# Optimization experiments

Measured on AMD Instinct MI355X. Metric: run time of the kernel, lower is better.

The kernel has to match this reference:

```python
import jax, jax.numpy as jnp
import numpy as np

B, N, F_IN = 4, 2048, 256
K, D = 4, 64
NEG_SLOPE = 0.2


def setup_inputs() -> dict:
    key = jax.random.key(0)
    k1, k2, k3, k4, k5 = jax.random.split(key, 5)
    x = jax.random.normal(k1, (B, N, F_IN), dtype=jnp.float32)
    adj = jax.random.randint(k2, (B, N, N), 0, 2, dtype=jnp.int32)
    # xavier_uniform-style params
    def xavier(k, shape):
        fan_in, fan_out = shape[-2], shape[-1]
        lim = np.sqrt(6.0 / (fan_in + fan_out))
        return jax.random.uniform(k, shape, jnp.float32, -lim, lim)
    W = xavier(k3, (K, F_IN, D))
    a_src = xavier(k4, (K, D, 1))
    a_dst = xavier(k5, (K, D, 1))
    return {"x": x, "adj": adj, "W": W, "a_src": a_src, "a_dst": a_dst}


def reference(x, adj, W, a_src, a_dst):
    # Wh: (B, K, N, D)
    Wh = jnp.einsum('bnf,kfd->bknd', x, W)
    e_src = jnp.einsum('bknd,kdo->bkno', Wh, a_src)  # (B,K,N,1)
    e_dst = jnp.einsum('bknd,kdo->bkno', Wh, a_dst)  # (B,K,N,1)
    e = e_src + jnp.swapaxes(e_dst, -2, -1)          # (B,K,N,N)
    e = jnp.where(e > 0, e, NEG_SLOPE * e)           # LeakyReLU(0.2)
    # adjacency mask with forced self-loops (adj + I > 0)
    eye = jnp.eye(e.shape[-1], dtype=bool)
    mask = (adj[:, None, :, :] > 0) | eye            # (B,1|K,N,N)
    e = jnp.where(mask, e, -jnp.inf)
    # numerically-stable softmax matching F_module_softmax
    x_max = jnp.max(e, axis=-1, keepdims=True)
    x_max = jnp.where(jnp.isinf(x_max), 0.0, x_max)
    exp_e = jnp.exp(e - x_max)
    exp_e = jnp.where(jnp.isinf(e), 0.0, exp_e)
    alpha = exp_e / (jnp.sum(exp_e, axis=-1, keepdims=True) + 1e-10)
    # dropout is identity in eval mode
    out = jnp.matmul(alpha, Wh)                      # (B,K,N,D)
    # concat heads: (B,N,K*D)
    Bn, Kn, Nn, Dn = out.shape
    return jnp.transpose(out, (0, 2, 1, 3)).reshape(Bn, Nn, Kn * Dn)
```

## Files before the change

kernel.cpp:

```cpp
#include <hip/hip_runtime.h>

#define NB 4
#define NN 2048
#define NF 256
#define NK 4
#define ND 64
#define NEG 0.2f
#define LOG2E 1.4426950408889634f

typedef _Float16 f16;
typedef _Float16 f16x2 __attribute__((ext_vector_type(2)));
typedef _Float16 f16x4 __attribute__((ext_vector_type(4)));
typedef _Float16 f16x8 __attribute__((ext_vector_type(8)));
typedef float f32x4 __attribute__((ext_vector_type(4)));
typedef float f32x16 __attribute__((ext_vector_type(16)));
typedef unsigned int u32;
typedef unsigned short u16;

__device__ __forceinline__ int gsz(int d) { return (d ^ (d >> 3)) & 7; }

__global__ __launch_bounds__(256) void k01(
    const float* __restrict__ x,
    const int*   __restrict__ adj,
    const float* __restrict__ Wm,
    const float* __restrict__ a_src,
    const float* __restrict__ a_dst,
    unsigned int* __restrict__ abit,
    f16* __restrict__ wht,
    float* __restrict__ sbuf,
    f16* __restrict__ ebuf,
    f16* __restrict__ fbuf)
{
    __shared__ f16 wt[64 * 256];

    const int bx  = blockIdx.x;
    const int tid = threadIdx.x;

    if (bx >= 256) {
        const int row = (bx - 256) * 4 + (tid >> 6);
        const int l   = tid & 63;
        const int i   = row & (NN - 1);
        const int* __restrict__ ar = adj + (size_t)row * NN;

        int v[32];
#pragma unroll
        for (int c = 0; c < 32; ++c) v[c] = ar[c * 64 + l];

        unsigned int kx = 0, ky = 0;
#pragma unroll
        for (int c = 0; c < 32; ++c) {
            unsigned long long m = __ballot(v[c] > 0);
            if (l == c) { kx = (unsigned int)m; ky = (unsigned int)(m >> 32); }
        }
        if (l == (i >> 6)) {
            unsigned int sb = 1u << (i & 31);
            if (((i >> 5) & 1) == 0) kx |= sb; else ky |= sb;
        }
        if (l < 32) {
            uint2 kk; kk.x = kx; kk.y = ky;
            *(uint2*)&abit[(size_t)row * 64 + l * 2] = kk;
        }
        return;
    }

    const int gx  = bx & 15;
    const int k   = (bx >> 4) & 3;
    const int b   = bx >> 6;
    const int wv  = tid >> 6;
    const int l   = tid & 63;
    const int q   = l >> 4;
    const int r16 = l & 15;

    for (int fc = 0; fc < 64; ++fc) {
        int f = fc * 4 + wv;
        int d = l;
        wt[d * 256 + (f ^ ((d & 7) << 3))] = (f16)Wm[(k * NF + f) * ND + d];
    }
    __syncthreads();

    const int ncol0 = gx * 128 + wv * 32;
    f32x4 acc[2][4];
#pragma unroll
    for (int nt = 0; nt < 2; ++nt)
#pragma unroll
        for (int dt = 0; dt < 4; ++dt)
            acc[nt][dt] = (f32x4){0.f, 0.f, 0.f, 0.f};

    for (int fs = 0; fs < 16; ++fs) {
        const int f0 = fs * 16 + q * 4;
        f16x4 af[4];
#pragma unroll
        for (int dt = 0; dt < 4; ++dt) {
            int d = dt * 16 + r16;
            af[dt] = *(const f16x4*)&wt[d * 256 + (f0 ^ ((d & 7) << 3))];
        }
#pragma unroll
        for (int nt = 0; nt < 2; ++nt) {
            int n = ncol0 + nt * 16 + r16;
            float4 xv = *(const float4*)&x[((size_t)(b * NN + n)) * NF + f0];
            f16x4 bf = {(f16)xv.x, (f16)xv.y, (f16)xv.z, (f16)xv.w};
#pragma unroll
            for (int dt = 0; dt < 4; ++dt)
                acc[nt][dt] = __builtin_amdgcn_mfma_f32_16x16x16f16(
                    af[dt], bf, acc[nt][dt], 0, 0, 0);
        }
    }

    float asv[4][4], adv[4][4];
#pragma unroll
    for (int dt = 0; dt < 4; ++dt)
#pragma unroll
        for (int rr = 0; rr < 4; ++rr) {
            int d = dt * 16 + q * 4 + rr;
            asv[dt][rr] = a_src[k * ND + d];
            adv[dt][rr] = a_dst[k * ND + d];
        }

    const size_t obase = (size_t)(b * NK + k) * 131072;

#pragma unroll
    for (int nt = 0; nt < 2; ++nt) {
        int n  = ncol0 + nt * 16 + r16;
        int s_ = n >> 6, g = (n >> 3) & 7, e = n & 7;
        float sp = 0.f, tp = 0.f;
#pragma unroll
        for (int dt = 0; dt < 4; ++dt)
#pragma unroll
            for (int rr = 0; rr < 4; ++rr) {
                float v = acc[nt][dt][rr];
                int d = dt * 16 + q * 4 + rr;
                wht[obase + s_ * 4096 + d * 64 + ((g ^ gsz(d)) << 3) + e] = (f16)v;
                sp += v * asv[dt][rr];
                tp += v * adv[dt][rr];
            }
        sp += __shfl_xor(sp, 16);
        sp += __shfl_xor(sp, 32);
        tp += __shfl_xor(tp, 16);
        tp += __shfl_xor(tp, 32);
        if (q == 0) {
            int idx = (b * NK + k) * NN + n;
            sbuf[idx] = sp;
            ebuf[idx] = (f16)__builtin_exp2f(tp * LOG2E);
            fbuf[idx] = (f16)__builtin_exp2f(0.2f * LOG2E * tp);
        }
    }
}

__global__ __launch_bounds__(512, 4) void k2_attn(
    const unsigned int* __restrict__ abit,
    const f16* __restrict__ wht,
    const float* __restrict__ sbuf,
    const f16* __restrict__ ebuf,
    const f16* __restrict__ fbuf,
    float* __restrict__ out)
{
    const int i0  = blockIdx.x * 64;
    const int k   = blockIdx.y;
    const int b   = blockIdx.z;
    const int tid = threadIdx.x;
    const int w   = tid >> 6;
    const int c   = w >> 1;
    const int rw  = w & 1;
    const int l   = tid & 63;
    const int r32 = l & 31;
    const int hi  = l >> 5;
    const int iglob = i0 + rw * 32 + r32;

    __shared__ __attribute__((aligned(16))) char pool[74752];
    u16*   el   = (u16*)(pool + 65536);
    u16*   fl   = (u16*)(pool + 69632);
    float* dden = (float*)(pool + 73728);

    const unsigned int* __restrict__ abrow =
        abit + (size_t)(b * NN + iglob) * 64 + c * 16;
    uint2 abx[8];
#pragma unroll
    for (int it = 0; it < 8; ++it) abx[it] = *(const uint2*)(abrow + it * 2);

    {
        const u16* eb = (const u16*)(ebuf + (b * NK + k) * NN);
        const u16* fb = (const u16*)(fbuf + (b * NK + k) * NN);
        *(ushort4*)&el[tid * 4] = *(const ushort4*)&eb[tid * 4];
        *(ushort4*)&fl[tid * 4] = *(const ushort4*)&fb[tid * 4];
    }

    const float s   = sbuf[(b * NK + k) * NN + iglob];
    const float Aff = __builtin_exp2f(0.8f * LOG2E * fminf(s, 0.f));
    const float Bff = __builtin_exp2f(-0.8f * LOG2E * fmaxf(s, 0.f));
    const f16 Afh = (f16)Aff, Bfh = (f16)Bff;
    const f16x2 Af2 = {Afh, Afh};
    const f16x2 Bf2 = {Bfh, Bfh};
    const f16x2 one2 = {(f16)1.0f, (f16)1.0f};
    const char* gtiles = (const char*)wht + (size_t)(b * NK + k) * 262144;

    float denom = 0.f;
    f32x16 acc[2];
#pragma unroll
    for (int dh = 0; dh < 2; ++dh)
#pragma unroll
        for (int z = 0; z < 16; ++z) acc[dh][z] = 0.f;

#define STAGE8(bb, it)                                                         \
    do {                                                                       \
        const char* gsrc = gtiles + (size_t)(c * 8 + (it)) * 8192 +            \
                           rw * 1024 + l * 16;                                 \
        char* ldst = pool + c * 16384 + (bb) * 8192 + rw * 1024 + l * 16;      \
        _Pragma("unroll") for (int kk = 0; kk < 4; ++kk)                       \
            __builtin_amdgcn_global_load_lds(                                  \
                (const __attribute__((address_space(1))) void*)(gsrc +         \
                    kk * 2048),                                                \
                (__attribute__((address_space(3))) void*)(ldst + kk * 2048),   \
                16, 0, 0);                                                     \
    } while (0)

    STAGE8(0, 0);

#pragma unroll
    for (int it = 0; it < 8; ++it) {
        asm volatile("s_waitcnt vmcnt(0) lgkmcnt(0)" ::: "memory");
        __builtin_amdgcn_sched_barrier(0);
        __builtin_amdgcn_s_barrier();
        __builtin_amdgcn_sched_barrier(0);
        if (it < 7) STAGE8((it + 1) & 1, it + 1);

        const char* lb = pool + c * 16384 + (it & 1) * 8192;
        const uint2 ab = abx[it];
#pragma unroll
        for (int jts = 0; jts < 4; ++jts) {
            const u32 word = (jts & 2) ? ab.y : ab.x;
            const u32 bbyte = (word >> (((jts & 1) << 4) + (hi << 3))) & 0xffu;
            const u32 u = bbyte * 0x8001u;
            const int jb = c * 512 + it * 64 + jts * 16 + hi * 8;
            uint4 E4 = *(const uint4*)&el[jb];
            uint4 F4 = *(const uint4*)&fl[jb];
            u32 pa_u[4];
#pragma unroll
            for (int p = 0; p < 4; ++p) {
                f16x2 e2 = __builtin_bit_cast(f16x2, ((const u32*)&E4)[p]);
                f16x2 f2 = __builtin_bit_cast(f16x2, ((const u32*)&F4)[p]);
                f16x2 w2 = __builtin_elementwise_max(Af2 * e2, Bf2 * f2);
                u32 x  = (u >> (2 * p)) & 0x00010001u;
                u32 mm = x * 0xffffu;
                u32 wu = __builtin_bit_cast(u32, w2) & mm;
                pa_u[p] = wu;
                denom = __builtin_amdgcn_fdot2(
                    __builtin_bit_cast(f16x2, wu), one2, denom, false);
            }
            uint4 pav = {pa_u[0], pa_u[1], pa_u[2], pa_u[3]};
            f16x8 pa = __builtin_bit_cast(f16x8, pav);
#pragma unroll
            for (int dh = 0; dh < 2; ++dh) {
                const int d = dh * 32 + r32;
                f16x8 v8 = *(const f16x8*)(lb + d * 128 +
                               ((((jts << 1) | hi) ^ gsz(d)) << 4));
                acc[dh] = __builtin_amdgcn_mfma_f32_32x32x16_f16(
                    pa, v8, acc[dh], 0, 0, 0);
            }
        }
    }
#undef STAGE8

    denom += __shfl_xor(denom, 32);

    __syncthreads();
    float* stash = (float*)pool;
    if (c != 0) {
        float* sb = stash + ((c - 1) * 2 + rw) * 2048 + l * 32;
#pragma unroll
        for (int dh = 0; dh < 2; ++dh)
#pragma unroll
            for (int sub = 0; sub < 4; ++sub) {
                f32x4 v = {acc[dh][sub * 4], acc[dh][sub * 4 + 1],
                           acc[dh][sub * 4 + 2], acc[dh][sub * 4 + 3]};
                *(f32x4*)&sb[dh * 16 + ((sub ^ (l & 3)) << 2)] = v;
            }
    }
    if (hi == 0) dden[c * 64 + rw * 32 + r32] = denom;
    __syncthreads();

    if (c == 0) {
#pragma unroll
        for (int cc = 0; cc < 3; ++cc) {
            const float* sr = stash + (cc * 2 + rw) * 2048 + l * 32;
#pragma unroll
            for (int dh = 0; dh < 2; ++dh)
#pragma unroll
                for (int sub = 0; sub < 4; ++sub) {
                    f32x4 v = *(const f32x4*)&sr[dh * 16 + ((sub ^ (l & 3)) << 2)];
#pragma unroll
                    for (int m = 0; m < 4; ++m) acc[dh][sub * 4 + m] += v[m];
                }
        }
        float* op = out + ((size_t)(b * NN) + i0 + rw * 32) * (NK * ND) + k * ND;
#pragma unroll
        for (int g4 = 0; g4 < 4; ++g4) {
            f32x4 ds = {0.f, 0.f, 0.f, 0.f};
#pragma unroll
            for (int c4 = 0; c4 < 4; ++c4) {
                f32x4 dv = *(const f32x4*)&dden[c4 * 64 + rw * 32 + g4 * 8 + hi * 4];
#pragma unroll
                for (int m = 0; m < 4; ++m) ds[m] += dv[m];
            }
#pragma unroll
            for (int m = 0; m < 4; ++m) {
                const int rr   = g4 * 4 + m;
                const int irow = g4 * 8 + hi * 4 + m;
                const float inv = 1.f / (ds[m] + 1e-10f);
                op[(size_t)irow * (NK * ND) + r32]      = acc[0][rr] * inv;
                op[(size_t)irow * (NK * ND) + 32 + r32] = acc[1][rr] * inv;
            }
        }
    }
}

extern "C" void kernel_launch(void* const* d_in, const int* in_sizes, int n_in,
                              void* d_out, int out_size, void* d_ws, size_t ws_size,
                              hipStream_t stream) {
    const float* x     = (const float*)d_in[0];
    const int*   adj   = (const int*)d_in[1];
    const float* Wm    = (const float*)d_in[2];
    const float* a_src = (const float*)d_in[3];
    const float* a_dst = (const float*)d_in[4];
    float* out = (float*)d_out;

    char* ws = (char*)d_ws;
    f16*   wht  = (f16*)ws;
    float* sbuf = (float*)(ws + (4u << 20));
    f16*   ebuf = (f16*)(ws + (4u << 20) + (128u << 10));
    f16*   fbuf = (f16*)(ws + (4u << 20) + (192u << 10));
    unsigned int* abit = (unsigned int*)(ws + (4u << 20) + (256u << 10));

    k01<<<dim3(256 + NB * NN / 4), 256, 0, stream>>>(
        x, adj, Wm, a_src, a_dst, abit, wht, sbuf, ebuf, fbuf);
    k2_attn<<<dim3(NN / 64, NK, NB), 512, 0, stream>>>(
        abit, wht, sbuf, ebuf, fbuf, out);
}
```

Measured before the change: 42.71 us.

## Split attention key range across all eight waves with per-wave pipelines and tree reduction

The attention kernel changes from 4 key-chunks × 2 row-halves to 8 waves that each own a 256-key slice and compute both 32-row tiles. Each V fragment loaded from LDS is now reused for two MFMAs. Each wave stages its own Wh tiles with a double-buffered global_load_lds pipeline using partial vmcnt waits, which removes the per-iteration workgroup barrier. The Wh tile layout and swizzle are changed to 32-column slabs to match, the grid is flattened so blocks sharing the same (b,k) run adjacently, and the cross-wave sum becomes a log-depth LDS tree reduction. The cost is more accumulator registers, because acc doubles, and a longer reduction epilogue.

```diff
diff --git a/kernel.cpp b/kernel.cpp
--- a/kernel.cpp
+++ b/kernel.cpp
@@ -17,7 +17,7 @@
 typedef unsigned int u32;
 typedef unsigned short u16;
 
-__device__ __forceinline__ int gsz(int d) { return (d ^ (d >> 3)) & 7; }
+__device__ __forceinline__ int gq(int d) { return ((d >> 1) ^ (d >> 3)) & 3; }
 
 __global__ __launch_bounds__(256) void k01(
     const float* __restrict__ x,
@@ -121,7 +121,7 @@
 #pragma unroll
     for (int nt = 0; nt < 2; ++nt) {
         int n  = ncol0 + nt * 16 + r16;
-        int s_ = n >> 6, g = (n >> 3) & 7, e = n & 7;
+        int s_ = n >> 5, g = (n >> 3) & 3, e = n & 7;
         float sp = 0.f, tp = 0.f;
 #pragma unroll
         for (int dt = 0; dt < 4; ++dt)
@@ -129,7 +129,7 @@
             for (int rr = 0; rr < 4; ++rr) {
                 float v = acc[nt][dt][rr];
                 int d = dt * 16 + q * 4 + rr;
-                wht[obase + s_ * 4096 + d * 64 + ((g ^ gsz(d)) << 3) + e] = (f16)v;
+                wht[obase + s_ * 2048 + d * 32 + ((g ^ gq(d)) << 3) + e] = (f16)v;
                 sp += v * asv[dt][rr];
                 tp += v * adv[dt][rr];
             }
@@ -154,163 +154,200 @@
     const f16* __restrict__ fbuf,
     float* __restrict__ out)
 {
-    const int i0  = blockIdx.x * 64;
-    const int k   = blockIdx.y;
-    const int b   = blockIdx.z;
+    const int bid = blockIdx.x;
+    const int bkv = (bid & 7) | (((bid >> 3) & 1) << 3);
+    const int rg  = bid >> 4;
+    const int b   = bkv >> 2, k = bkv & 3;
     const int tid = threadIdx.x;
     const int w   = tid >> 6;
-    const int c   = w >> 1;
-    const int rw  = w & 1;
     const int l   = tid & 63;
     const int r32 = l & 31;
     const int hi  = l >> 5;
-    const int iglob = i0 + rw * 32 + r32;
-
-    __shared__ __attribute__((aligned(16))) char pool[74752];
+    const int rowbase = rg * 64;
+
+    __shared__ __attribute__((aligned(16))) char pool[76032];
     u16*   el   = (u16*)(pool + 65536);
     u16*   fl   = (u16*)(pool + 69632);
     float* dden = (float*)(pool + 73728);
-
-    const unsigned int* __restrict__ abrow =
-        abit + (size_t)(b * NN + iglob) * 64 + c * 16;
-    uint2 abx[8];
-#pragma unroll
-    for (int it = 0; it < 8; ++it) abx[it] = *(const uint2*)(abrow + it * 2);
+    float* dsum = (float*)(pool + 75776);
+
+    const unsigned int* ab0 = abit + (size_t)(b * NN + rowbase + r32) * 64 + w * 8;
+    const unsigned int* ab1 = ab0 + 32 * 64;
+    uint2 abxA[4], abxB[4];
+#pragma unroll
+    for (int xw = 0; xw < 4; ++xw) {
+        abxA[xw] = *(const uint2*)(ab0 + xw * 2);
+        abxB[xw] = *(const uint2*)(ab1 + xw * 2);
+    }
+    const float s0 = sbuf[bkv * NN + rowbase + r32];
+    const float s1 = sbuf[bkv * NN + rowbase + 32 + r32];
 
     {
-        const u16* eb = (const u16*)(ebuf + (b * NK + k) * NN);
-        const u16* fb = (const u16*)(fbuf + (b * NK + k) * NN);
-        *(ushort4*)&el[tid * 4] = *(const ushort4*)&eb[tid * 4];
-        *(ushort4*)&fl[tid * 4] = *(const ushort4*)&fb[tid * 4];
-    }
-
-    const float s   = sbuf[(b * NK + k) * NN + iglob];
-    const float Aff = __builtin_exp2f(0.8f * LOG2E * fminf(s, 0.f));
-    const float Bff = __builtin_exp2f(-0.8f * LOG2E * fmaxf(s, 0.f));
-    const f16 Afh = (f16)Aff, Bfh = (f16)Bff;
-    const f16x2 Af2 = {Afh, Afh};
-    const f16x2 Bf2 = {Bfh, Bfh};
+        const u16* eb = (const u16*)(ebuf + bkv * NN);
+        const u16* fb = (const u16*)(fbuf + bkv * NN);
+        *(uint2*)&el[tid * 4] = *(const uint2*)&eb[tid * 4];
+        *(uint2*)&fl[tid * 4] = *(const uint2*)&fb[tid * 4];
+    }
+
+    const f16 Af0h = (f16)__builtin_exp2f(0.8f * LOG2E * fminf(s0, 0.f));
+    const f16 Bf0h = (f16)__builtin_exp2f(-0.8f * LOG2E * fmaxf(s0, 0.f));
+    const f16 Af1h = (f16)__builtin_exp2f(0.8f * LOG2E * fminf(s1, 0.f));
+    const f16 Bf1h = (f16)__builtin_exp2f(-0.8f * LOG2E * fmaxf(s1, 0.f));
+    const f16x2 Af2[2] = {{Af0h, Af0h}, {Af1h, Af1h}};
+    const f16x2 Bf2[2] = {{Bf0h, Bf0h}, {Bf1h, Bf1h}};
     const f16x2 one2 = {(f16)1.0f, (f16)1.0f};
-    const char* gtiles = (const char*)wht + (size_t)(b * NK + k) * 262144;
-
-    float denom = 0.f;
-    f32x16 acc[2];
-#pragma unroll
-    for (int dh = 0; dh < 2; ++dh)
-#pragma unroll
-        for (int z = 0; z < 16; ++z) acc[dh][z] = 0.f;
-
-#define STAGE8(bb, it)                                                         \
+    const char* gtb = (const char*)wht + (size_t)bkv * 262144;
+
+    const int G0 = ((r32 >> 1) ^ (r32 >> 3)) & 3;
+    const int G1 = (((32 + r32) >> 1) ^ ((32 + r32) >> 3)) & 3;
+    const int fb0 = r32 * 64;
+    const int fb1 = 2048 + r32 * 64;
+
+    float den0 = 0.f, den1 = 0.f;
+    f32x16 acc[2][2];
+#pragma unroll
+    for (int rt = 0; rt < 2; ++rt)
+#pragma unroll
+        for (int dh = 0; dh < 2; ++dh)
+#pragma unroll
+            for (int z = 0; z < 16; ++z) acc[rt][dh][z] = 0.f;
+
+#define STAGE(bb, it)                                                          \
     do {                                                                       \
-        const char* gsrc = gtiles + (size_t)(c * 8 + (it)) * 8192 +            \
-                           rw * 1024 + l * 16;                                 \
-        char* ldst = pool + c * 16384 + (bb) * 8192 + rw * 1024 + l * 16;      \
+        const char* gsrc = gtb + (size_t)(w * 8 + (it)) * 4096 + l * 16;       \
+        char* ldst = pool + w * 8192 + (bb) * 4096;                            \
         _Pragma("unroll") for (int kk = 0; kk < 4; ++kk)                       \
             __builtin_amdgcn_global_load_lds(                                  \
                 (const __attribute__((address_space(1))) void*)(gsrc +         \
-                    kk * 2048),                                                \
-                (__attribute__((address_space(3))) void*)(ldst + kk * 2048),   \
+                    kk * 1024),                                                \
+                (__attribute__((address_space(3))) void*)(ldst + kk * 1024),   \
                 16, 0, 0);                                                     \
     } while (0)
 
-    STAGE8(0, 0);
+    STAGE(0, 0);
+    STAGE(1, 1);
+    __syncthreads();
 
 #pragma unroll
     for (int it = 0; it < 8; ++it) {
-        asm volatile("s_waitcnt vmcnt(0) lgkmcnt(0)" ::: "memory");
+        if (it < 7) asm volatile("s_waitcnt vmcnt(4)" ::: "memory");
+        else        asm volatile("s_waitcnt vmcnt(0)" ::: "memory");
         __builtin_amdgcn_sched_barrier(0);
-        __builtin_amdgcn_s_barrier();
+
+        const char* lb = pool + w * 8192 + (it & 1) * 4096;
+        const int j0 = w * 256 + it * 32;
+        const u32 wordA = (it & 1) ? abxA[it >> 1].y : abxA[it >> 1].x;
+        const u32 wordB = (it & 1) ? abxB[it >> 1].y : abxB[it >> 1].x;
+
+#pragma unroll
+        for (int jts = 0; jts < 2; ++jts) {
+            const int v = (jts << 1) | hi;
+            uint4 E4 = *(const uint4*)&el[j0 + jts * 16 + hi * 8];
+            uint4 F4 = *(const uint4*)&fl[j0 + jts * 16 + hi * 8];
+            f16x8 v8_0 = *(const f16x8*)(lb + fb0 + ((v ^ G0) << 4));
+            f16x8 v8_1 = *(const f16x8*)(lb + fb1 + ((v ^ G1) << 4));
+
+            f16x8 pa[2];
+#pragma unroll
+            for (int rt = 0; rt < 2; ++rt) {
+                const u32 word = rt ? wordB : wordA;
+                const u32 bbyte = (word >> ((jts << 4) + (hi << 3))) & 0xffu;
+                const u32 u = bbyte * 0x8001u;
+                u32 pa_u[4];
+#pragma unroll
+                for (int p = 0; p < 4; ++p) {
+                    f16x2 e2 = __builtin_bit_cast(f16x2, ((const u32*)&E4)[p]);
+                    f16x2 f2 = __builtin_bit_cast(f16x2, ((const u32*)&F4)[p]);
+                    f16x2 w2 = __builtin_elementwise_max(Af2[rt] * e2,
+                                                         Bf2[rt] * f2);
+                    u32 mm = ((u >> (2 * p)) & 0x00010001u) * 0xffffu;
+                    u32 wu = __builtin_bit_cast(u32, w2) & mm;
+                    pa_u[p] = wu;
+                    float& dref = rt ? den1 : den0;
+                    dref = __builtin_amdgcn_fdot2(
+                        __builtin_bit_cast(f16x2, wu), one2, dref, false);
+                }
+                uint4 pav = {pa_u[0], pa_u[1], pa_u[2], pa_u[3]};
+                pa[rt] = __builtin_bit_cast(f16x8, pav);
+            }
+            acc[0][0] = __builtin_amdgcn_mfma_f32_32x32x16_f16(pa[0], v8_0,
+                                                               acc[0][0], 0, 0, 0);
+            acc[0][1] = __builtin_amdgcn_mfma_f32_32x32x16_f16(pa[0], v8_1,
+                                                               acc[0][1], 0, 0, 0);
+            acc[1][0] = __builtin_amdgcn_mfma_f32_32x32x16_f16(pa[1], v8_0,
+                                                               acc[1][0], 0, 0, 0);
+            acc[1][1] = __builtin_amdgcn_mfma_f32_32x32x16_f16(pa[1], v8_1,
+                                                               acc[1][1], 0, 0, 0);
+        }
+        asm volatile("s_waitcnt lgkmcnt(0)" ::: "memory");
         __builtin_amdgcn_sched_barrier(0);
-        if (it < 7) STAGE8((it + 1) & 1, it + 1);
-
-        const char* lb = pool + c * 16384 + (it & 1) * 8192;
-        const uint2 ab = abx[it];
-#pragma unroll
-        for (int jts = 0; jts < 4; ++jts) {
-            const u32 word = (jts & 2) ? ab.y : ab.x;
-            const u32 bbyte = (word >> (((jts & 1) << 4) + (hi << 3))) & 0xffu;
-            const u32 u = bbyte * 0x8001u;
-            const int jb = c * 512 + it * 64 + jts * 16 + hi * 8;
-            uint4 E4 = *(const uint4*)&el[jb];
-            uint4 F4 = *(const uint4*)&fl[jb];
-            u32 pa_u[4];
-#pragma unroll
-            for (int p = 0; p < 4; ++p) {
-                f16x2 e2 = __builtin_bit_cast(f16x2, ((const u32*)&E4)[p]);
-                f16x2 f2 = __builtin_bit_cast(f16x2, ((const u32*)&F4)[p]);
-                f16x2 w2 = __builtin_elementwise_max(Af2 * e2, Bf2 * f2);
-                u32 x  = (u >> (2 * p)) & 0x00010001u;
-                u32 mm = x * 0xffffu;
-                u32 wu = __builtin_bit_cast(u32, w2) & mm;
-                pa_u[p] = wu;
-                denom = __builtin_amdgcn_fdot2(
-                    __builtin_bit_cast(f16x2, wu), one2, denom, false);
-            }
-            uint4 pav = {pa_u[0], pa_u[1], pa_u[2], pa_u[3]};
-            f16x8 pa = __builtin_bit_cast(f16x8, pav);
-#pragma unroll
-            for (int dh = 0; dh < 2; ++dh) {
-                const int d = dh * 32 + r32;
-                f16x8 v8 = *(const f16x8*)(lb + d * 128 +
-                               ((((jts << 1) | hi) ^ gsz(d)) << 4));
-                acc[dh] = __builtin_amdgcn_mfma_f32_32x32x16_f16(
-                    pa, v8, acc[dh], 0, 0, 0);
-            }
-        }
-    }
-#undef STAGE8
-
-    denom += __shfl_xor(denom, 32);
-
-    __syncthreads();
-    float* stash = (float*)pool;
-    if (c != 0) {
-        float* sb = stash + ((c - 1) * 2 + rw) * 2048 + l * 32;
-#pragma unroll
-        for (int dh = 0; dh < 2; ++dh)
-#pragma unroll
-            for (int sub = 0; sub < 4; ++sub) {
-                f32x4 v = {acc[dh][sub * 4], acc[dh][sub * 4 + 1],
-                           acc[dh][sub * 4 + 2], acc[dh][sub * 4 + 3]};
-                *(f32x4*)&sb[dh * 16 + ((sub ^ (l & 3)) << 2)] = v;
-            }
-    }
-    if (hi == 0) dden[c * 64 + rw * 32 + r32] = denom;
-    __syncthreads();
-
-    if (c == 0) {
-#pragma unroll
-        for (int cc = 0; cc < 3; ++cc) {
-            const float* sr = stash + (cc * 2 + rw) * 2048 + l * 32;
-#pragma unroll
-            for (int dh = 0; dh < 2; ++dh)
-#pragma unroll
-                for (int sub = 0; sub < 4; ++sub) {
-                    f32x4 v = *(const f32x4*)&sr[dh * 16 + ((sub ^ (l & 3)) << 2)];
-#pragma unroll
-                    for (int m = 0; m < 4; ++m) acc[dh][sub * 4 + m] += v[m];
+        if (it < 6) STAGE(it & 1, it + 2);
+    }
+#undef STAGE
+
+    den0 += __shfl_xor(den0, 32);
+    den1 += __shfl_xor(den1, 32);
+    if (hi == 0) {
+        dden[w * 64 + r32]      = den0;
+        dden[w * 64 + 32 + r32] = den1;
+    }
+
+#define TDUMP(reg)                                                             \
+    do {                                                                       \
+        float* rb = (float*)(pool + (reg) * 16384) + l * 64;                   \
+        _Pragma("unroll") for (int rt = 0; rt < 2; ++rt)                       \
+        _Pragma("unroll") for (int dh = 0; dh < 2; ++dh)                       \
+        _Pragma("unroll") for (int sub = 0; sub < 4; ++sub) {                  \
+            f32x4 vv = {acc[rt][dh][sub * 4], acc[rt][dh][sub * 4 + 1],        \
+                        acc[rt][dh][sub * 4 + 2], acc[rt][dh][sub * 4 + 3]};   \
+            *(f32x4*)&rb[((rt * 8 + dh * 4 + sub) ^ (l & 15)) << 2] = vv;      \
+        }                                                                      \
+    } while (0)
+#define TADD(reg)                                                              \
+    do {                                                                       \
+        const float* rb = (const float*)(pool + (reg) * 16384) + l * 64;       \
+        _Pragma("unroll") for (int rt = 0; rt < 2; ++rt)                       \
+        _Pragma("unroll") for (int dh = 0; dh < 2; ++dh)                       \
+        _Pragma("unroll") for (int sub = 0; sub < 4; ++sub) {                  \
+            f32x4 vv = *(const f32x4*)                                         \
+                &rb[((rt * 8 + dh * 4 + sub) ^ (l & 15)) << 2];                \
+            _Pragma("unroll") for (int m = 0; m < 4; ++m)                      \
+                acc[rt][dh][sub * 4 + m] += vv[m];                             \
+        }                                                                      \
+    } while (0)
+
+    __syncthreads();
+    if (w >= 4) TDUMP(w - 4);
+    __syncthreads();
+    if (w < 4) TADD(w);
+    if (w == 2 || w == 3) TDUMP(w);
+    __syncthreads();
+    if (w < 2) TADD(w + 2);
+    if (w == 1) TDUMP(1);
+    __syncthreads();
+    if (w == 0) {
+        TADD(1);
+        float dd8 = 0.f;
+#pragma unroll
+        for (int ww = 0; ww < 8; ++ww) dd8 += dden[ww * 64 + l];
+        dsum[l] = dd8;
+        float* ob = out + ((size_t)(b * NN) + rowbase) * (NK * ND) + k * ND;
+#pragma unroll
+        for (int rt = 0; rt < 2; ++rt)
+#pragma unroll
+            for (int g4 = 0; g4 < 4; ++g4)
+#pragma unroll
+                for (int m = 0; m < 4; ++m) {
+                    const int rowl = rt * 32 + g4 * 8 + hi * 4 + m;
+                    const float inv = 1.f / (dsum[rowl] + 1e-10f);
+                    const int rr = g4 * 4 + m;
+                    ob[(size_t)rowl * (NK * ND) + r32] = acc[rt][0][rr] * inv;
+                    ob[(size_t)rowl * (NK * ND) + 32 + r32] =
+                        acc[rt][1][rr] * inv;
                 }
-        }
-        float* op = out + ((size_t)(b * NN) + i0 + rw * 32) * (NK * ND) + k * ND;
-#pragma unroll
-        for (int g4 = 0; g4 < 4; ++g4) {
-            f32x4 ds = {0.f, 0.f, 0.f, 0.f};
-#pragma unroll
-            for (int c4 = 0; c4 < 4; ++c4) {
-                f32x4 dv = *(const f32x4*)&dden[c4 * 64 + rw * 32 + g4 * 8 + hi * 4];
-#pragma unroll
-                for (int m = 0; m < 4; ++m) ds[m] += dv[m];
-            }
-#pragma unroll
-            for (int m = 0; m < 4; ++m) {
-                const int rr   = g4 * 4 + m;
-                const int irow = g4 * 8 + hi * 4 + m;
-                const float inv = 1.f / (ds[m] + 1e-10f);
-                op[(size_t)irow * (NK * ND) + r32]      = acc[0][rr] * inv;
-                op[(size_t)irow * (NK * ND) + 32 + r32] = acc[1][rr] * inv;
-            }
-        }
-    }
+    }
+#undef TDUMP
+#undef TADD
 }
 
 extern "C" void kernel_launch(void* const* d_in, const int* in_sizes, int n_in,
@@ -332,6 +369,6 @@
 
     k01<<<dim3(256 + NB * NN / 4), 256, 0, stream>>>(
         x, adj, Wm, a_src, a_dst, abit, wht, sbuf, ebuf, fbuf);
-    k2_attn<<<dim3(NN / 64, NK, NB), 512, 0, stream>>>(
+    k2_attn<<<dim3(512), 512, 0, stream>>>(
         abit, wht, sbuf, ebuf, fbuf, out);
 }
```

After: 68.47 us. +60.3%, slower.

## Compute softmax denominator via MFMA with ones and remap grid to 1D

Applied to the files above, without the earlier changes.

Replaces the per-element fdot2 denominator accumulation with an extra MFMA against a ones matrix, so row sums come out in the accumulator layout and the separate denominator LDS buffer and shuffle go away. The attention kernel grid becomes 1D, with block IDs interleaving the 16 (batch, head) pairs fastest so that concurrently resident blocks spread across heads and batches. It also simplifies the mask construction with shifts and stashes the denominator tile alongside the partial accumulators. The cost is one more MFMA per step and a larger stash in shared memory.

```diff
diff --git a/kernel.cpp b/kernel.cpp
--- a/kernel.cpp
+++ b/kernel.cpp
@@ -154,9 +154,11 @@
     const f16* __restrict__ fbuf,
     float* __restrict__ out)
 {
-    const int i0  = blockIdx.x * 64;
-    const int k   = blockIdx.y;
-    const int b   = blockIdx.z;
+    const int bid = blockIdx.x;
+    const int bkv = (bid & 7) | (((bid >> 3) & 1) << 3);
+    const int rg  = bid >> 4;
+    const int b   = bkv >> 2, k = bkv & 3;
+    const int i0  = rg * 64;
     const int tid = threadIdx.x;
     const int w   = tid >> 6;
     const int c   = w >> 1;
@@ -167,9 +169,8 @@
     const int iglob = i0 + rw * 32 + r32;
 
     __shared__ __attribute__((aligned(16))) char pool[74752];
-    u16*   el   = (u16*)(pool + 65536);
-    u16*   fl   = (u16*)(pool + 69632);
-    float* dden = (float*)(pool + 73728);
+    u16* el = (u16*)(pool + 65536);
+    u16* fl = (u16*)(pool + 69632);
 
     const unsigned int* __restrict__ abrow =
         abit + (size_t)(b * NN + iglob) * 64 + c * 16;
@@ -178,27 +179,24 @@
     for (int it = 0; it < 8; ++it) abx[it] = *(const uint2*)(abrow + it * 2);
 
     {
-        const u16* eb = (const u16*)(ebuf + (b * NK + k) * NN);
-        const u16* fb = (const u16*)(fbuf + (b * NK + k) * NN);
+        const u16* eb = (const u16*)(ebuf + bkv * NN);
+        const u16* fb = (const u16*)(fbuf + bkv * NN);
         *(ushort4*)&el[tid * 4] = *(const ushort4*)&eb[tid * 4];
         *(ushort4*)&fl[tid * 4] = *(const ushort4*)&fb[tid * 4];
     }
 
-    const float s   = sbuf[(b * NK + k) * NN + iglob];
-    const float Aff = __builtin_exp2f(0.8f * LOG2E * fminf(s, 0.f));
-    const float Bff = __builtin_exp2f(-0.8f * LOG2E * fmaxf(s, 0.f));
-    const f16 Afh = (f16)Aff, Bfh = (f16)Bff;
+    const float s   = sbuf[bkv * NN + iglob];
+    const f16 Afh = (f16)__builtin_exp2f(0.8f * LOG2E * fminf(s, 0.f));
+    const f16 Bfh = (f16)__builtin_exp2f(-0.8f * LOG2E * fmaxf(s, 0.f));
     const f16x2 Af2 = {Afh, Afh};
     const f16x2 Bf2 = {Bfh, Bfh};
-    const f16x2 one2 = {(f16)1.0f, (f16)1.0f};
-    const char* gtiles = (const char*)wht + (size_t)(b * NK + k) * 262144;
-
-    float denom = 0.f;
-    f32x16 acc[2];
-#pragma unroll
-    for (int dh = 0; dh < 2; ++dh)
-#pragma unroll
-        for (int z = 0; z < 16; ++z) acc[dh][z] = 0.f;
+    const f16 h1 = (f16)1.0f;
+    const f16x8 ones8 = {h1, h1, h1, h1, h1, h1, h1, h1};
+    const char* gtiles = (const char*)wht + (size_t)bkv * 262144;
+
+    f32x16 acc[2], accd;
+#pragma unroll
+    for (int z = 0; z < 16; ++z) { acc[0][z] = 0.f; acc[1][z] = 0.f; accd[z] = 0.f; }
 
 #define STAGE8(bb, it)                                                         \
     do {                                                                       \
@@ -229,7 +227,7 @@
         for (int jts = 0; jts < 4; ++jts) {
             const u32 word = (jts & 2) ? ab.y : ab.x;
             const u32 bbyte = (word >> (((jts & 1) << 4) + (hi << 3))) & 0xffu;
-            const u32 u = bbyte * 0x8001u;
+            const u32 u = (bbyte << 15) | bbyte;
             const int jb = c * 512 + it * 64 + jts * 16 + hi * 8;
             uint4 E4 = *(const uint4*)&el[jb];
             uint4 F4 = *(const uint4*)&fl[jb];
@@ -240,11 +238,8 @@
                 f16x2 f2 = __builtin_bit_cast(f16x2, ((const u32*)&F4)[p]);
                 f16x2 w2 = __builtin_elementwise_max(Af2 * e2, Bf2 * f2);
                 u32 x  = (u >> (2 * p)) & 0x00010001u;
-                u32 mm = x * 0xffffu;
-                u32 wu = __builtin_bit_cast(u32, w2) & mm;
-                pa_u[p] = wu;
-                denom = __builtin_amdgcn_fdot2(
-                    __builtin_bit_cast(f16x2, wu), one2, denom, false);
+                u32 mm = (x << 16) - x;
+                pa_u[p] = __builtin_bit_cast(u32, w2) & mm;
             }
             uint4 pav = {pa_u[0], pa_u[1], pa_u[2], pa_u[3]};
             f16x8 pa = __builtin_bit_cast(f16x8, pav);
@@ -256,16 +251,15 @@
                 acc[dh] = __builtin_amdgcn_mfma_f32_32x32x16_f16(
                     pa, v8, acc[dh], 0, 0, 0);
             }
+            accd = __builtin_amdgcn_mfma_f32_32x32x16_f16(pa, ones8, accd, 0, 0, 0);
         }
     }
 #undef STAGE8
-
-    denom += __shfl_xor(denom, 32);
 
     __syncthreads();
     float* stash = (float*)pool;
     if (c != 0) {
-        float* sb = stash + ((c - 1) * 2 + rw) * 2048 + l * 32;
+        float* sb = stash + ((c - 1) * 2 + rw) * 3072 + l * 48;
 #pragma unroll
         for (int dh = 0; dh < 2; ++dh)
 #pragma unroll
@@ -274,14 +268,19 @@
                            acc[dh][sub * 4 + 2], acc[dh][sub * 4 + 3]};
                 *(f32x4*)&sb[dh * 16 + ((sub ^ (l & 3)) << 2)] = v;
             }
-    }
-    if (hi == 0) dden[c * 64 + rw * 32 + r32] = denom;
+#pragma unroll
+        for (int sub = 0; sub < 4; ++sub) {
+            f32x4 v = {accd[sub * 4], accd[sub * 4 + 1],
+                       accd[sub * 4 + 2], accd[sub * 4 + 3]};
+            *(f32x4*)&sb[32 + ((sub ^ (l & 3)) << 2)] = v;
+        }
+    }
     __syncthreads();
 
     if (c == 0) {
 #pragma unroll
         for (int cc = 0; cc < 3; ++cc) {
-            const float* sr = stash + (cc * 2 + rw) * 2048 + l * 32;
+            const float* sr = stash + (cc * 2 + rw) * 3072 + l * 48;
 #pragma unroll
             for (int dh = 0; dh < 2; ++dh)
 #pragma unroll
@@ -290,26 +289,24 @@
 #pragma unroll
                     for (int m = 0; m < 4; ++m) acc[dh][sub * 4 + m] += v[m];
                 }
+#pragma unroll
+            for (int sub = 0; sub < 4; ++sub) {
+                f32x4 v = *(const f32x4*)&sr[32 + ((sub ^ (l & 3)) << 2)];
+#pragma unroll
+                for (int m = 0; m < 4; ++m) accd[sub * 4 + m] += v[m];
+            }
         }
         float* op = out + ((size_t)(b * NN) + i0 + rw * 32) * (NK * ND) + k * ND;
 #pragma unroll
-        for (int g4 = 0; g4 < 4; ++g4) {
-            f32x4 ds = {0.f, 0.f, 0.f, 0.f};
-#pragma unroll
-            for (int c4 = 0; c4 < 4; ++c4) {
-                f32x4 dv = *(const f32x4*)&dden[c4 * 64 + rw * 32 + g4 * 8 + hi * 4];
-#pragma unroll
-                for (int m = 0; m < 4; ++m) ds[m] += dv[m];
-            }
+        for (int g4 = 0; g4 < 4; ++g4)
 #pragma unroll
             for (int m = 0; m < 4; ++m) {
                 const int rr   = g4 * 4 + m;
                 const int irow = g4 * 8 + hi * 4 + m;
-                const float inv = 1.f / (ds[m] + 1e-10f);
+                const float inv = 1.f / (accd[rr] + 1e-10f);
                 op[(size_t)irow * (NK * ND) + r32]      = acc[0][rr] * inv;
                 op[(size_t)irow * (NK * ND) + 32 + r32] = acc[1][rr] * inv;
             }
-        }
     }
 }
 
@@ -332,6 +329,6 @@
 
     k01<<<dim3(256 + NB * NN / 4), 256, 0, stream>>>(
         x, adj, Wm, a_src, a_dst, abit, wht, sbuf, ebuf, fbuf);
-    k2_attn<<<dim3(NN / 64, NK, NB), 512, 0, stream>>>(
+    k2_attn<<<dim3(512), 512, 0, stream>>>(
         abit, wht, sbuf, ebuf, fbuf, out);
 }
```

After: 41.99 us. About the same (-1.7%).
